# Performance work log

Hardware: AMD Instinct MI355X
Metric: run time of the kernel (lower is better)

The kernel has to match this reference:

```python
import jax, jax.numpy as jnp
import numpy as np

B, C, H, W = 8, 128, 64, 64
KC = 32  # key_channels

def setup_inputs() -> dict:
    key = jax.random.key(0)
    ks = jax.random.split(key, 6)
    s = lambda fan_in: 1.0 / np.sqrt(fan_in)
    x  = jax.random.normal(ks[0], (B, C, H, W), dtype=jnp.float32)
    Wq = jax.random.uniform(ks[1], (KC, C), jnp.float32, -s(C), s(C))  # 1x1 conv kernels
    Wk = jax.random.uniform(ks[2], (KC, C), jnp.float32, -s(C), s(C))
    Wv = jax.random.uniform(ks[3], (C, C), jnp.float32, -s(C), s(C))
    Wo = jax.random.uniform(ks[4], (C, C), jnp.float32, -s(C), s(C))
    gamma = jnp.zeros((1,), jnp.float32) + 0.1  # nonzero so attention path matters
    return {"x": x, "Wq": Wq, "Wk": Wk, "Wv": Wv, "Wo": Wo, "gamma": gamma}

def reference(x, Wq, Wk, Wv, Wo, gamma):
    b, c, h, w = x.shape
    xf = x.reshape(b, c, h * w)                      # [B,C,N]
    Q = jnp.einsum('qc,bcn->bnq', Wq, xf)            # [B,N,KC]
    K = jnp.einsum('kc,bcn->bkn', Wk, xf)            # [B,KC,N]
    V = jnp.einsum('vc,bcn->bnv', Wv, xf)            # [B,N,C]
    scores = jnp.einsum('bnq,bqm->bnm', Q, K) / jnp.sqrt(jnp.asarray(Wq.shape[0], x.dtype))
    attn = jax.nn.softmax(scores, axis=-1)           # [B,N,N]
    out = jnp.einsum('bnm,bmv->bvn', attn, V)        # [B,C,N]
    out = jnp.einsum('oc,bcn->bon', Wo, out).reshape(b, c, h, w)
    return x + gamma * out
```

## Files before the change

### kernel.cpp

```cpp
#include <hip/hip_runtime.h>
#include <hip/hip_bf16.h>

#define BB 8
#define CC 128
#define NN 4096
#define KCQ 32

typedef unsigned short u16;
typedef unsigned int u32;
typedef unsigned char u8;
typedef __bf16 bf16x8 __attribute__((ext_vector_type(8)));
typedef float f32x4 __attribute__((ext_vector_type(4)));
typedef long i64;
typedef long i64x2 __attribute__((ext_vector_type(2)));

typedef const __attribute__((address_space(1))) void gas_t;
typedef __attribute__((address_space(3))) void las_t;

__device__ __forceinline__ u16 f2bf(float f){
  u32 u = __builtin_bit_cast(u32, f);
  u32 r = u + 0x7FFFu + ((u >> 16) & 1u);
  return (u16)(r >> 16);
}
__device__ __forceinline__ u32 cvtpk(float lo, float hi){
  u32 r; asm("v_cvt_pk_bf16_f32 %0, %1, %2" : "=v"(r) : "v"(lo), "v"(hi)); return r;
}
__device__ __forceinline__ u32 pk_fp8x4(float a, float b, float c, float d){
  int v = 0;
  v = __builtin_amdgcn_cvt_pk_fp8_f32(a, b, v, false);
  v = __builtin_amdgcn_cvt_pk_fp8_f32(c, d, v, true);
  return (u32)v;
}
__device__ __forceinline__ void gload16(const void* g, void* l){
  __builtin_amdgcn_global_load_lds((gas_t*)g, (las_t*)l, 16, 0, 0);
}

__global__ __launch_bounds__(256) void k_prep_w(const float* Wq, const float* Wk,
                                                const float* Wv, const float* Wo,
                                                u16* wsq, u16* wsk, u16* wsv, u16* wso){
  int i = blockIdx.x * 256 + threadIdx.x;
  const float SC = 0.2550350f;
  if (i < 4096)       wsq[i]        = f2bf(Wq[i] * SC);
  else if (i < 8192)  wsk[i-4096]   = f2bf(Wk[i-4096]);
  else if (i < 24576) wsv[i-8192]   = f2bf(Wv[i-8192]);
  else if (i < 40960) wso[i-24576]  = f2bf(Wo[i-24576]);
}

__global__ __launch_bounds__(512) void k_projx(const float* x, const u16* wq, const u16* wk,
                                               const u16* wv, u16* Qm, u16* Km, u8* Vt8){
  __shared__ __align__(16) u16 xL[64*132];
  int b = blockIdx.x >> 6, nb = (blockIdx.x & 63) * 64;
  int t = threadIdx.x;
  int n = t & 63, cg = t >> 6;
  #pragma unroll
  for (int it = 0; it < 16; ++it){
    int c = it*8 + cg;
    xL[n*132 + c] = f2bf(x[((size_t)b*CC + c)*NN + nb + n]);
  }
  __syncthreads();
  int w = t >> 6, l = t & 63, a = l & 15, g = l >> 4;
  int ns = w >> 1, half = w & 1;
  int n0 = nb + ns*16;
  bf16x8 xa[4];
  #pragma unroll
  for (int kc = 0; kc < 4; ++kc)
    xa[kc] = *(const bf16x8*)(xL + (ns*16 + a)*132 + kc*32 + g*8);
  __syncthreads();

  u32* vbuf = (u32*)xL;
  auto Vjob = [&](int vt){
    f32x4 acc = {0.f,0.f,0.f,0.f};
    #pragma unroll
    for (int kc = 0; kc < 4; ++kc){
      bf16x8 wa = ((const bf16x8*)(wv + (size_t)(vt*16 + a) * CC))[kc*4 + g];
      acc = __builtin_amdgcn_mfma_f32_16x16x32_bf16(xa[kc], wa, acc, 0,0,0);
    }
    int row = vt*16 + a;
    vbuf[row*16 + ((ns ^ ((a>>1)&3)) << 2) + g] = pk_fp8x4(acc[0], acc[1], acc[2], acc[3]);
  };

  if (half == 0){
    #pragma unroll
    for (int qt = 0; qt < 2; ++qt){
      f32x4 accq = {0.f,0.f,0.f,0.f}, acck = {0.f,0.f,0.f,0.f};
      #pragma unroll
      for (int kc = 0; kc < 4; ++kc){
        bf16x8 wbq = ((const bf16x8*)(wq + (size_t)(qt*16 + a) * CC))[kc*4 + g];
        bf16x8 wbk = ((const bf16x8*)(wk + (size_t)(qt*16 + a) * CC))[kc*4 + g];
        accq = __builtin_amdgcn_mfma_f32_16x16x32_bf16(xa[kc], wbq, accq, 0,0,0);
        acck = __builtin_amdgcn_mfma_f32_16x16x32_bf16(xa[kc], wbk, acck, 0,0,0);
      }
      #pragma unroll
      for (int r = 0; r < 4; ++r){
        Qm[((size_t)b*NN + n0 + 4*g + r) * KCQ + qt*16 + a] = f2bf(accq[r]);
        Km[((size_t)b*NN + n0 + 4*g + r) * KCQ + qt*16 + a] = f2bf(acck[r]);
      }
    }
    Vjob(0); Vjob(1);
  } else {
    #pragma unroll
    for (int vt = 2; vt < 8; ++vt) Vjob(vt);
  }
  __syncthreads();
  {
    int row = t >> 2, gg = t & 3, key = (row >> 1) & 3;
    const u32* vb = vbuf + row*16;
    auto rd = [&](int d){ return vb[(((d>>2)^key)<<2) + (d&3)]; };
    uint4 dd;
    dd.x = rd(2*gg);     dd.y = rd(2*gg+1);
    dd.z = rd(8+2*gg);   dd.w = rd(9+2*gg);
    *(uint4*)(Vt8 + ((size_t)b*CC + row)*NN + nb + gg*16) = dd;
  }
}

__global__ __launch_bounds__(512, 4) void k_attn(const u16* Qm, const u16* Km,
                                                 const u8* Vt8, const u16* wso,
                                                 const float* x, const float* gamma,
                                                 float* out){
  __shared__ __align__(16) char smem[65536];
  int bid = blockIdx.x;
  int b = bid & 7, qb = bid >> 3;
  int t0 = threadIdx.x;
  int l = t0 & 63, a = l & 15, g = l >> 4;
  int w = t0 >> 6, h = w >> 2, wq = w & 3;
  int q0 = qb * 64;
  int kb0 = h * 2048;

  const u8* Vb = Vt8 + (size_t)b * CC * NN;

  bf16x8 qf[4];
  #pragma unroll
  for (int qs = 0; qs < 4; ++qs)
    qf[qs] = ((const bf16x8*)(Qm + ((size_t)b*NN + q0 + qs*16 + a) * KCQ))[g];
  const u16* kPtr = Km + ((size_t)b*NN + kb0 + wq*16 + a) * KCQ + g*8;

  f32x4 o[8];
  #pragma unroll
  for (int i = 0; i < 8; ++i) o[i] = (f32x4){0.f,0.f,0.f,0.f};
  float ls[4] = {0.f, 0.f, 0.f, 0.f};

  int schk = (l&3) ^ ((l>>3)&3);
  const u8* vSrc = Vb + (size_t)(wq*32 + (l>>2))*NN + kb0 + (schk << 4);
  const int vOff = h*8192 + wq*2048 + l*16;
  auto stageV = [&](int t1, int sl){
    const u8* vs = vSrc + t1*64;
    char* vd = smem + sl*16384 + vOff;
    gload16(vs, vd);
    gload16(vs + (size_t)16*NN, vd + 1024);
  };

  const int cswz = (a >> 1) & 3;
  const int rc = (g ^ cswz) << 4;
  auto PV = [&](int ps, int vsl){
    const char* Vs = smem + vsl*16384 + h*8192;
    const char* Pr = smem + 49152 + ps*8192 + h*4096;
    __builtin_amdgcn_s_setprio(1);
    i64x2 vf0 = *(const i64x2*)(Vs + (wq*32 + a)*64 + rc);
    i64x2 vf1 = *(const i64x2*)(Vs + (wq*32 + 16 + a)*64 + rc);
    #pragma unroll
    for (int qs = 0; qs < 4; ++qs){
      i64x2 pf = *(const i64x2*)(Pr + (qs*16 + a)*64 + rc);
      o[qs*2  ] = __builtin_amdgcn_mfma_f32_16x16x32_fp8_fp8(vf0[0], pf[0], o[qs*2  ], 0,0,0);
      o[qs*2  ] = __builtin_amdgcn_mfma_f32_16x16x32_fp8_fp8(vf0[1], pf[1], o[qs*2  ], 0,0,0);
      o[qs*2+1] = __builtin_amdgcn_mfma_f32_16x16x32_fp8_fp8(vf1[0], pf[0], o[qs*2+1], 0,0,0);
      o[qs*2+1] = __builtin_amdgcn_mfma_f32_16x16x32_fp8_fp8(vf1[1], pf[1], o[qs*2+1], 0,0,0);
    }
    __builtin_amdgcn_s_setprio(0);
  };

  const int ppos = (((((wq&1)<<1) | (g>>1)) ^ cswz) << 4) | ((wq>>1) << 3) | ((g&1) << 2);
  auto SM = [&](const f32x4* sv, char* Pw){
    #pragma unroll
    for (int qs = 0; qs < 4; ++qs){
      float p0 = __builtin_amdgcn_exp2f(sv[qs][0]);
      float p1 = __builtin_amdgcn_exp2f(sv[qs][1]);
      float p2 = __builtin_amdgcn_exp2f(sv[qs][2]);
      float p3 = __builtin_amdgcn_exp2f(sv[qs][3]);
      ls[qs] += (p0 + p1) + (p2 + p3);
      *(u32*)(Pw + (qs*16 + a)*64 + ppos) = pk_fp8x4(p0, p1, p2, p3);
    }
  };

  char* PwBase = smem + 49152 + h*4096;

  bf16x8 kfC = *(const bf16x8*)(kPtr);
  bf16x8 kfN = *(const bf16x8*)(kPtr + 2048);
  stageV(0, 0);
  stageV(1, 1);
  {
    f32x4 sv[4];
    #pragma unroll
    for (int qs = 0; qs < 4; ++qs){
      f32x4 z = {0.f,0.f,0.f,0.f};
      sv[qs] = __builtin_amdgcn_mfma_f32_16x16x32_bf16(kfC, qf[qs], z, 0,0,0);
    }
    SM(sv, PwBase);
  }
  asm volatile("s_waitcnt vmcnt(2) lgkmcnt(0)" ::: "memory");
  __builtin_amdgcn_s_barrier();

  int vR = 0;
  for (int t = 0; t < 31; ++t){
    f32x4 sv[4];
    #pragma unroll
    for (int qs = 0; qs < 4; ++qs){
      f32x4 z = {0.f,0.f,0.f,0.f};
      sv[qs] = __builtin_amdgcn_mfma_f32_16x16x32_bf16(kfN, qf[qs], z, 0,0,0);
    }
    PV(t & 1, vR);
    SM(sv, PwBase + ((t+1)&1)*8192);
    if (t < 30){
      kfC = *(const bf16x8*)(kPtr + (size_t)(t+2)*2048);
      int sl = vR >= 1 ? vR - 1 : 2;
      stageV(t+2, sl);
      asm volatile("s_waitcnt vmcnt(3) lgkmcnt(0)" ::: "memory");
    } else {
      asm volatile("s_waitcnt vmcnt(0) lgkmcnt(0)" ::: "memory");
    }
    __builtin_amdgcn_s_barrier();
    kfN = kfC;
    vR = (vR == 2) ? 0 : vR + 1;
  }
  PV(1, vR);

  #pragma unroll
  for (int qs = 0; qs < 4; ++qs){
    ls[qs] += __shfl_xor(ls[qs], 16);
    ls[qs] += __shfl_xor(ls[qs], 32);
  }
  float* Ml = (float*)(smem + 36864);
  if (l < 16){
    #pragma unroll
    for (int qs = 0; qs < 4; ++qs) Ml[w*64 + qs*16 + l] = ls[qs];
  }
  float* Cx = (float*)smem;
  __syncthreads();
  if (h == 1){
    #pragma unroll
    for (int i = 0; i < 8; ++i){
      int qs = i >> 1, st = i & 1;
      *(f32x4*)(Cx + (qs*16 + a)*132 + wq*32 + st*16 + 4*g) = o[i];
    }
  }
  __syncthreads();
  u16* Ol = (u16*)(smem + 49152);
  if (h == 0){
    #pragma unroll
    for (int qs = 0; qs < 4; ++qs){
      float lsum = 0.f;
      #pragma unroll
      for (int ww = 0; ww < 8; ++ww) lsum += Ml[ww*64 + qs*16 + a];
      float inv = 1.f / lsum;
      #pragma unroll
      for (int st = 0; st < 2; ++st){
        f32x4 oc = o[qs*2 + st];
        const float* cx = Cx + (qs*16 + a)*132 + wq*32 + st*16 + 4*g;
        uint2 pk;
        pk.x = cvtpk((oc[0] + cx[0]) * inv, (oc[1] + cx[1]) * inv);
        pk.y = cvtpk((oc[2] + cx[2]) * inv, (oc[3] + cx[3]) * inv);
        int chunk = (wq*4 + st*2 + (g>>1)) ^ (a & 7);
        *(uint2*)((char*)Ol + (qs*16 + a)*256 + chunk*16 + (g&1)*8) = pk;
      }
    }
  }
  __syncthreads();
  float gm = gamma[0];
  f32x4 acc2[4];
  #pragma unroll
  for (int qs = 0; qs < 4; ++qs) acc2[qs] = (f32x4){0.f,0.f,0.f,0.f};
  #pragma unroll
  for (int kc = 0; kc < 4; ++kc){
    bf16x8 wof = *(const bf16x8*)(wso + (size_t)(w*16 + a)*CC + kc*32 + g*8);
    #pragma unroll
    for (int qs = 0; qs < 4; ++qs){
      int chunk = (kc*4 + g) ^ (a & 7);
      bf16x8 of = *(const bf16x8*)((const char*)Ol + (qs*16 + a)*256 + chunk*16);
      acc2[qs] = __builtin_amdgcn_mfma_f32_16x16x32_bf16(wof, of, acc2[qs], 0,0,0);
    }
  }
  #pragma unroll
  for (int qs = 0; qs < 4; ++qs){
    #pragma unroll
    for (int r = 0; r < 4; ++r){
      size_t idx = ((size_t)b*CC + w*16 + 4*g + r)*NN + q0 + qs*16 + a;
      out[idx] = x[idx] + gm * acc2[qs][r];
    }
  }
}

extern "C" void kernel_launch(void* const* d_in, const int* in_sizes, int n_in,
                              void* d_out, int out_size, void* d_ws, size_t ws_size,
                              hipStream_t stream) {
  const float* x     = (const float*)d_in[0];
  const float* Wq    = (const float*)d_in[1];
  const float* Wk    = (const float*)d_in[2];
  const float* Wv    = (const float*)d_in[3];
  const float* Wo    = (const float*)d_in[4];
  const float* gamma = (const float*)d_in[5];
  float* out = (float*)d_out;

  u16* wsq = (u16*)d_ws;
  u16* wsk = wsq + 4096;
  u16* wsv = wsk + 4096;
  u16* wso = wsv + 16384;
  u16* Qm  = wso + 16384;
  u16* Km  = Qm + (size_t)BB*NN*KCQ;
  u8*  Vt8 = (u8*)(Km + (size_t)BB*NN*KCQ);

  hipLaunchKernelGGL(k_prep_w, dim3(160), dim3(256), 0, stream, Wq, Wk, Wv, Wo, wsq, wsk, wsv, wso);
  hipLaunchKernelGGL(k_projx,  dim3(512), dim3(512), 0, stream, x, wsq, wsk, wsv, Qm, Km, Vt8);
  hipLaunchKernelGGL(k_attn,   dim3(512), dim3(512), 0, stream, Qm, Km, Vt8, wso, x, gamma, out);
}
```

Measured before the change: 68.70 us.

## Restructure attention split so each wave owns 16 V channels over full keys

The attention kernel stops splitting the key range between two wave halves. Each of the 8 waves now covers all keys in 128-key tiles and owns 16 output channels, with double-buffered V/P tiles instead of a triple buffer. This removes the cross-half partial-output merge through shared memory and cuts shared memory from 64 KB to 48 KB, which may raise occupancy. In exchange there are fewer, larger pipeline stages with only two buffers, so there is less latency hiding. Separately, the projection kernel stages Wv into shared memory rather than reading it from global memory for each MFMA.

```diff
diff --git a/kernel.cpp b/kernel.cpp
--- a/kernel.cpp
+++ b/kernel.cpp
@@ -49,6 +49,7 @@
 __global__ __launch_bounds__(512) void k_projx(const float* x, const u16* wq, const u16* wk,
                                                const u16* wv, u16* Qm, u16* Km, u8* Vt8){
   __shared__ __align__(16) u16 xL[64*132];
+  __shared__ __align__(16) u16 wvL[128*132];
   int b = blockIdx.x >> 6, nb = (blockIdx.x & 63) * 64;
   int t = threadIdx.x;
   int n = t & 63, cg = t >> 6;
@@ -56,6 +57,13 @@
   for (int it = 0; it < 16; ++it){
     int c = it*8 + cg;
     xL[n*132 + c] = f2bf(x[((size_t)b*CC + c)*NN + nb + n]);
+  }
+  {
+    int r = t >> 2, c0 = (t & 3) * 32;
+    const u32* src = (const u32*)wv + r*64 + (t&3)*16;
+    #pragma unroll
+    for (int j = 0; j < 16; ++j)
+      *(u32*)(wvL + r*132 + c0 + j*2) = src[j];
   }
   __syncthreads();
   int w = t >> 6, l = t & 63, a = l & 15, g = l >> 4;
@@ -72,7 +80,7 @@
     f32x4 acc = {0.f,0.f,0.f,0.f};
     #pragma unroll
     for (int kc = 0; kc < 4; ++kc){
-      bf16x8 wa = ((const bf16x8*)(wv + (size_t)(vt*16 + a) * CC))[kc*4 + g];
+      bf16x8 wa = *(const bf16x8*)(wvL + (vt*16 + a)*132 + kc*32 + g*8);
       acc = __builtin_amdgcn_mfma_f32_16x16x32_bf16(xa[kc], wa, acc, 0,0,0);
     }
     int row = vt*16 + a;
@@ -117,14 +125,13 @@
                                                  const u8* Vt8, const u16* wso,
                                                  const float* x, const float* gamma,
                                                  float* out){
-  __shared__ __align__(16) char smem[65536];
+  __shared__ __align__(16) char smem[49152];
   int bid = blockIdx.x;
   int b = bid & 7, qb = bid >> 3;
   int t0 = threadIdx.x;
   int l = t0 & 63, a = l & 15, g = l >> 4;
-  int w = t0 >> 6, h = w >> 2, wq = w & 3;
+  int w = t0 >> 6;
   int q0 = qb * 64;
-  int kb0 = h * 2048;
 
   const u8* Vb = Vt8 + (size_t)b * CC * NN;
 
@@ -132,43 +139,25 @@
   #pragma unroll
   for (int qs = 0; qs < 4; ++qs)
     qf[qs] = ((const bf16x8*)(Qm + ((size_t)b*NN + q0 + qs*16 + a) * KCQ))[g];
-  const u16* kPtr = Km + ((size_t)b*NN + kb0 + wq*16 + a) * KCQ + g*8;
-
-  f32x4 o[8];
-  #pragma unroll
-  for (int i = 0; i < 8; ++i) o[i] = (f32x4){0.f,0.f,0.f,0.f};
+  const u16* kPtr = Km + ((size_t)b*NN + w*16 + a) * KCQ + g*8;
+
+  f32x4 o[4];
+  #pragma unroll
+  for (int i = 0; i < 4; ++i) o[i] = (f32x4){0.f,0.f,0.f,0.f};
   float ls[4] = {0.f, 0.f, 0.f, 0.f};
 
-  int schk = (l&3) ^ ((l>>3)&3);
-  const u8* vSrc = Vb + (size_t)(wq*32 + (l>>2))*NN + kb0 + (schk << 4);
-  const int vOff = h*8192 + wq*2048 + l*16;
-  auto stageV = [&](int t1, int sl){
-    const u8* vs = vSrc + t1*64;
-    char* vd = smem + sl*16384 + vOff;
-    gload16(vs, vd);
-    gload16(vs + (size_t)16*NN, vd + 1024);
+  int srcCh = ((l&7) ^ ((l>>3)&7)) << 4;
+  const u8* vS0 = Vb + (size_t)(w*16 + (l>>3))*NN + srcCh;
+  const u8* vS1 = vS0 + (size_t)8*NN;
+  const int vOff = w*2048 + l*16;
+  auto stageV = [&](int kt, int sl){
+    char* bs = smem + (sl << 14);
+    gload16(vS0 + kt*128, bs + vOff);
+    gload16(vS1 + kt*128, bs + vOff + 1024);
   };
 
-  const int cswz = (a >> 1) & 3;
-  const int rc = (g ^ cswz) << 4;
-  auto PV = [&](int ps, int vsl){
-    const char* Vs = smem + vsl*16384 + h*8192;
-    const char* Pr = smem + 49152 + ps*8192 + h*4096;
-    __builtin_amdgcn_s_setprio(1);
-    i64x2 vf0 = *(const i64x2*)(Vs + (wq*32 + a)*64 + rc);
-    i64x2 vf1 = *(const i64x2*)(Vs + (wq*32 + 16 + a)*64 + rc);
-    #pragma unroll
-    for (int qs = 0; qs < 4; ++qs){
-      i64x2 pf = *(const i64x2*)(Pr + (qs*16 + a)*64 + rc);
-      o[qs*2  ] = __builtin_amdgcn_mfma_f32_16x16x32_fp8_fp8(vf0[0], pf[0], o[qs*2  ], 0,0,0);
-      o[qs*2  ] = __builtin_amdgcn_mfma_f32_16x16x32_fp8_fp8(vf0[1], pf[1], o[qs*2  ], 0,0,0);
-      o[qs*2+1] = __builtin_amdgcn_mfma_f32_16x16x32_fp8_fp8(vf1[0], pf[0], o[qs*2+1], 0,0,0);
-      o[qs*2+1] = __builtin_amdgcn_mfma_f32_16x16x32_fp8_fp8(vf1[1], pf[1], o[qs*2+1], 0,0,0);
-    }
-    __builtin_amdgcn_s_setprio(0);
-  };
-
-  const int ppos = (((((wq&1)<<1) | (g>>1)) ^ cswz) << 4) | ((wq>>1) << 3) | ((g&1) << 2);
+  const int Cg = ((w>>2)<<2) | ((w&1)<<1) | (g>>1);
+  const int ppos = ((Cg ^ (a&7)) << 4) | (((w>>1)&1) << 3) | ((g&1) << 2);
   auto SM = [&](const f32x4* sv, char* Pw){
     #pragma unroll
     for (int qs = 0; qs < 4; ++qs){
@@ -177,91 +166,92 @@
       float p2 = __builtin_amdgcn_exp2f(sv[qs][2]);
       float p3 = __builtin_amdgcn_exp2f(sv[qs][3]);
       ls[qs] += (p0 + p1) + (p2 + p3);
-      *(u32*)(Pw + (qs*16 + a)*64 + ppos) = pk_fp8x4(p0, p1, p2, p3);
+      *(u32*)(Pw + (qs*16 + a)*128 + ppos) = pk_fp8x4(p0, p1, p2, p3);
     }
   };
 
-  char* PwBase = smem + 49152 + h*4096;
-
-  bf16x8 kfC = *(const bf16x8*)(kPtr);
-  bf16x8 kfN = *(const bf16x8*)(kPtr + 2048);
+  const int rc0 = (g ^ (a&7)) << 4;
+  const int rc1 = ((4 + g) ^ (a&7)) << 4;
+  auto PV = [&](int sl){
+    const char* Vs = smem + (sl << 14);
+    const char* Pr = smem + 32768 + (sl << 13);
+    __builtin_amdgcn_s_setprio(1);
+    i64x2 vf0 = *(const i64x2*)(Vs + (w*16 + a)*128 + rc0);
+    i64x2 vf1 = *(const i64x2*)(Vs + (w*16 + a)*128 + rc1);
+    #pragma unroll
+    for (int qs = 0; qs < 4; ++qs){
+      i64x2 pf0 = *(const i64x2*)(Pr + (qs*16 + a)*128 + rc0);
+      i64x2 pf1 = *(const i64x2*)(Pr + (qs*16 + a)*128 + rc1);
+      o[qs] = __builtin_amdgcn_mfma_f32_16x16x32_fp8_fp8(vf0[0], pf0[0], o[qs], 0,0,0);
+      o[qs] = __builtin_amdgcn_mfma_f32_16x16x32_fp8_fp8(vf0[1], pf0[1], o[qs], 0,0,0);
+      o[qs] = __builtin_amdgcn_mfma_f32_16x16x32_fp8_fp8(vf1[0], pf1[0], o[qs], 0,0,0);
+      o[qs] = __builtin_amdgcn_mfma_f32_16x16x32_fp8_fp8(vf1[1], pf1[1], o[qs], 0,0,0);
+    }
+    __builtin_amdgcn_s_setprio(0);
+  };
+
   stageV(0, 0);
-  stageV(1, 1);
+  bf16x8 kfB = *(const bf16x8*)kPtr;
+  bf16x8 kfA = *(const bf16x8*)(kPtr + 4096);
   {
     f32x4 sv[4];
     #pragma unroll
     for (int qs = 0; qs < 4; ++qs){
       f32x4 z = {0.f,0.f,0.f,0.f};
-      sv[qs] = __builtin_amdgcn_mfma_f32_16x16x32_bf16(kfC, qf[qs], z, 0,0,0);
-    }
-    SM(sv, PwBase);
-  }
-  asm volatile("s_waitcnt vmcnt(2) lgkmcnt(0)" ::: "memory");
+      sv[qs] = __builtin_amdgcn_mfma_f32_16x16x32_bf16(kfB, qf[qs], z, 0,0,0);
+    }
+    SM(sv, smem + 32768);
+  }
+  asm volatile("s_waitcnt vmcnt(0) lgkmcnt(0)" ::: "memory");
   __builtin_amdgcn_s_barrier();
-
-  int vR = 0;
+  kfB = kfA;
+
   for (int t = 0; t < 31; ++t){
+    stageV(t+1, (t+1)&1);
     f32x4 sv[4];
     #pragma unroll
     for (int qs = 0; qs < 4; ++qs){
       f32x4 z = {0.f,0.f,0.f,0.f};
-      sv[qs] = __builtin_amdgcn_mfma_f32_16x16x32_bf16(kfN, qf[qs], z, 0,0,0);
-    }
-    PV(t & 1, vR);
-    SM(sv, PwBase + ((t+1)&1)*8192);
+      sv[qs] = __builtin_amdgcn_mfma_f32_16x16x32_bf16(kfB, qf[qs], z, 0,0,0);
+    }
+    PV(t & 1);
+    SM(sv, smem + 32768 + (((t+1)&1) << 13));
     if (t < 30){
-      kfC = *(const bf16x8*)(kPtr + (size_t)(t+2)*2048);
-      int sl = vR >= 1 ? vR - 1 : 2;
-      stageV(t+2, sl);
-      asm volatile("s_waitcnt vmcnt(3) lgkmcnt(0)" ::: "memory");
+      kfA = *(const bf16x8*)(kPtr + (size_t)(t+2)*4096);
+      asm volatile("s_waitcnt vmcnt(1) lgkmcnt(0)" ::: "memory");
     } else {
       asm volatile("s_waitcnt vmcnt(0) lgkmcnt(0)" ::: "memory");
     }
     __builtin_amdgcn_s_barrier();
-    kfN = kfC;
-    vR = (vR == 2) ? 0 : vR + 1;
-  }
-  PV(1, vR);
+    kfB = kfA;
+  }
+  PV(1);
 
   #pragma unroll
   for (int qs = 0; qs < 4; ++qs){
     ls[qs] += __shfl_xor(ls[qs], 16);
     ls[qs] += __shfl_xor(ls[qs], 32);
   }
-  float* Ml = (float*)(smem + 36864);
+  __syncthreads();
+  float* Ml = (float*)smem;
   if (l < 16){
     #pragma unroll
     for (int qs = 0; qs < 4; ++qs) Ml[w*64 + qs*16 + l] = ls[qs];
   }
-  float* Cx = (float*)smem;
-  __syncthreads();
-  if (h == 1){
-    #pragma unroll
-    for (int i = 0; i < 8; ++i){
-      int qs = i >> 1, st = i & 1;
-      *(f32x4*)(Cx + (qs*16 + a)*132 + wq*32 + st*16 + 4*g) = o[i];
-    }
-  }
-  __syncthreads();
-  u16* Ol = (u16*)(smem + 49152);
-  if (h == 0){
-    #pragma unroll
-    for (int qs = 0; qs < 4; ++qs){
-      float lsum = 0.f;
-      #pragma unroll
-      for (int ww = 0; ww < 8; ++ww) lsum += Ml[ww*64 + qs*16 + a];
-      float inv = 1.f / lsum;
-      #pragma unroll
-      for (int st = 0; st < 2; ++st){
-        f32x4 oc = o[qs*2 + st];
-        const float* cx = Cx + (qs*16 + a)*132 + wq*32 + st*16 + 4*g;
-        uint2 pk;
-        pk.x = cvtpk((oc[0] + cx[0]) * inv, (oc[1] + cx[1]) * inv);
-        pk.y = cvtpk((oc[2] + cx[2]) * inv, (oc[3] + cx[3]) * inv);
-        int chunk = (wq*4 + st*2 + (g>>1)) ^ (a & 7);
-        *(uint2*)((char*)Ol + (qs*16 + a)*256 + chunk*16 + (g&1)*8) = pk;
-      }
-    }
+  __syncthreads();
+  u16* Ol = (u16*)(smem + 4096);
+  #pragma unroll
+  for (int qs = 0; qs < 4; ++qs){
+    float lsum = 0.f;
+    #pragma unroll
+    for (int ww = 0; ww < 8; ++ww) lsum += Ml[ww*64 + qs*16 + a];
+    float inv = 1.f / lsum;
+    f32x4 oc = o[qs];
+    uint2 pk;
+    pk.x = cvtpk(oc[0]*inv, oc[1]*inv);
+    pk.y = cvtpk(oc[2]*inv, oc[3]*inv);
+    int chunk = (w*2 + (g>>1)) ^ (a & 7);
+    *(uint2*)((char*)Ol + (qs*16 + a)*256 + chunk*16 + (g&1)*8) = pk;
   }
   __syncthreads();
   float gm = gamma[0];
```

New measurement: 64.16 us. 6.6% less time.
